# Performance work log

Measured on AMD Instinct MI355X. Metric: run time of the kernel, lower is better.

## Reference

```python
import jax, jax.numpy as jnp
import numpy as np

D_IN = 1024
D_OUT = 1024
N = 4096


def setup_inputs() -> dict:
    key = jax.random.key(0)
    kx, kq, kk, kv = jax.random.split(key, 4)
    x = jax.random.normal(kx, (N, D_IN), dtype=jnp.float32)
    # weights stored as [d_in, d_out] so that x @ W == torch Linear(x)
    s = 1.0 / np.sqrt(D_IN)
    W_q = jax.random.uniform(kq, (D_IN, D_OUT), jnp.float32, -s, s)
    W_k = jax.random.uniform(kk, (D_IN, D_OUT), jnp.float32, -s, s)
    W_v = jax.random.uniform(kv, (D_IN, D_OUT), jnp.float32, -s, s)
    return {"x": x, "W_q": W_q, "W_k": W_k, "W_v": W_v}


def reference(x, W_q, W_k, W_v):
    # x: [N, d_in]; projections -> [N, d_out]
    q = x @ W_q
    k = x @ W_k
    v = x @ W_v
    scale = 1.0 / jnp.sqrt(jnp.asarray(k.shape[-1], dtype=q.dtype))
    scores = (q @ k.T) * scale            # [N, N]
    weights = jax.nn.softmax(scores, axis=-1)
    return weights @ v                     # [N, d_out]
```

## Files before the change

### kernel.cpp

```cpp
#include <hip/hip_runtime.h>
#include <math.h>

typedef _Float16 f16;
typedef __attribute__((ext_vector_type(8))) _Float16 f16x8;
typedef __attribute__((ext_vector_type(4))) _Float16 f16x4;
typedef __attribute__((ext_vector_type(4))) float f32x4;

#define NSEQ 4096
#define DIN 1024
#define DOUT 1024

__device__ __forceinline__ void load16(const void* g, void* l) {
    __builtin_amdgcn_global_load_lds(
        (const __attribute__((address_space(1))) unsigned int*)g,
        (__attribute__((address_space(3))) unsigned int*)l, 16, 0, 0);
}

template <typename OutT, int ESUM>
__global__ __launch_bounds__(256, 2)
void gemm_bt(const f16* __restrict__ A, const f16* __restrict__ B,
             OutT* __restrict__ c0, OutT* __restrict__ c1,
             OutT* __restrict__ c2, OutT* __restrict__ c3,
             int M, int N, int K, int lda, int ldb, int ldc, float scale,
             long aStrideZ, long bStrideZ,
             f16* __restrict__ TC, int tz, int ldt, float* __restrict__ Sums)
{
    const int z = blockIdx.z;
    A += (long)z * aStrideZ;
    B += (long)z * bStrideZ;
    OutT* C = z == 0 ? c0 : (z == 1 ? c1 : (z == 2 ? c2 : c3));
    __shared__ f16 As[2 * 128 * 32];
    __shared__ f16 Bs[2 * 128 * 32];

    int gx = gridDim.x;
    int bid = blockIdx.y * gx + blockIdx.x;
    int xcd = bid & 7, s = bid >> 3;
    int px = s & 7, rest = s >> 3;
    int py = rest & 3, chunk = rest >> 2;
    int pg = xcd + (chunk << 3);
    int pcols = gx >> 3;
    int lp = 31 - __clz(pcols);
    int bx = ((pg & (pcols - 1)) << 3) + px;
    int by = ((pg >> lp) << 2) + py;

    const int t    = threadIdx.x;
    const int lane = t & 63;
    const int wave = t >> 6;
    const int wm   = (wave >> 1) * 64;
    const int wn   = (wave & 1) * 64;
    const int tile_m = by * 128;
    const int tile_n = bx * 128;
    const int quad = lane >> 4;
    const int l16  = lane & 15;
    const int srow = t >> 2;
    const int scol = ((t & 3) ^ (srow & 3)) * 8;
    const int qx8 = (quad ^ (l16 & 3)) * 8;

    f32x4 acc[4][4];
#pragma unroll
    for (int i = 0; i < 4; i++)
#pragma unroll
        for (int j = 0; j < 4; j++)
            acc[i][j] = (f32x4){0.f, 0.f, 0.f, 0.f};

    const f16* Ab = A + (long)(tile_m + srow) * lda + scol;
    const f16* Bb = B + (long)(tile_n + srow) * ldb + scol;
    f16* Asd = As + t * 8;
    f16* Bsd = Bs + t * 8;

    for (int k0 = 0; k0 < K; k0 += 64) {
        load16(Ab + k0, Asd);
        load16(Ab + (long)64 * lda + k0, Asd + 2048);
        load16(Ab + k0 + 32, Asd + 4096);
        load16(Ab + (long)64 * lda + k0 + 32, Asd + 4096 + 2048);
        load16(Bb + k0, Bsd);
        load16(Bb + (long)64 * ldb + k0, Bsd + 2048);
        load16(Bb + k0 + 32, Bsd + 4096);
        load16(Bb + (long)64 * ldb + k0 + 32, Bsd + 4096 + 2048);
        __syncthreads();
#pragma unroll
        for (int p = 0; p < 2; p++) {
            f16x8 a[4], b[4];
#pragma unroll
            for (int i = 0; i < 4; i++)
                a[i] = *(const f16x8*)(As + p * 4096 + (wm + i * 16 + l16) * 32 + qx8);
#pragma unroll
            for (int j = 0; j < 4; j++)
                b[j] = *(const f16x8*)(Bs + p * 4096 + (wn + j * 16 + l16) * 32 + qx8);
#pragma unroll
            for (int i = 0; i < 4; i++)
#pragma unroll
                for (int j = 0; j < 4; j++)
                    acc[i][j] = __builtin_amdgcn_mfma_f32_16x16x32_f16(
                        a[i], b[j], acc[i][j], 0, 0, 0);
        }
        __syncthreads();
    }
    if (TC != nullptr && z == tz) {
#pragma unroll
        for (int i = 0; i < 4; i++)
#pragma unroll
            for (int j = 0; j < 4; j++) {
                f16x4 o;
#pragma unroll
                for (int r = 0; r < 4; r++) o[r] = (f16)(acc[i][j][r] * scale);
                int row0 = tile_m + wm + i * 16 + quad * 4;
                int col  = tile_n + wn + j * 16 + l16;
                *(f16x4*)(TC + (long)col * ldt + row0) = o;
            }
    } else if (ESUM) {
        const int bxs = bx * 2 + (wn >> 6);
#pragma unroll
        for (int i = 0; i < 4; i++) {
            float rs[4] = {0.f, 0.f, 0.f, 0.f};
#pragma unroll
            for (int j = 0; j < 4; j++)
#pragma unroll
                for (int r = 0; r < 4; r++) {
                    float e = __expf(acc[i][j][r] * scale);
                    int row = tile_m + wm + i * 16 + quad * 4 + r;
                    int col = tile_n + wn + j * 16 + l16;
                    C[(long)row * ldc + col] = (OutT)e;
                    rs[r] += e;
                }
#pragma unroll
            for (int msk = 1; msk < 16; msk <<= 1)
#pragma unroll
                for (int r = 0; r < 4; r++)
                    rs[r] += __shfl_xor(rs[r], msk, 64);
            if (l16 == 0)
#pragma unroll
                for (int r = 0; r < 4; r++) {
                    int row = tile_m + wm + i * 16 + quad * 4 + r;
                    Sums[(long)row * 64 + bxs] = rs[r];
                }
        }
    } else {
#pragma unroll
        for (int i = 0; i < 4; i++)
#pragma unroll
            for (int j = 0; j < 4; j++)
#pragma unroll
                for (int r = 0; r < 4; r++) {
                    int row = tile_m + wm + i * 16 + quad * 4 + r;
                    int col = tile_n + wn + j * 16 + l16;
                    C[(long)row * ldc + col] = (OutT)(acc[i][j][r] * scale);
                }
    }
}

__global__ void prep(const float* __restrict__ x,
                     const float* __restrict__ W0, const float* __restrict__ W1,
                     const float* __restrict__ W2,
                     f16* __restrict__ xb, f16* __restrict__ Wt) {
    if (blockIdx.z == 3) {
        long base = ((long)(blockIdx.y * 16 + blockIdx.x) * 256 + threadIdx.x) * 4;
#pragma unroll
        for (int it = 0; it < 16; it++) {
            long i = base + (long)it * (256 * 256 * 4);
            f32x4 v = *(const f32x4*)(x + i);
            f16x4 o;
            o.x = (f16)v.x; o.y = (f16)v.y; o.z = (f16)v.z; o.w = (f16)v.w;
            *(f16x4*)(xb + i) = o;
        }
        return;
    }
    __shared__ f16 tile[64][65];
    const float* W = blockIdx.z == 0 ? W0 : (blockIdx.z == 1 ? W1 : W2);
    f16* O = Wt + (long)blockIdx.z * DIN * DOUT;
    int r0 = blockIdx.y * 64;
    int c0 = blockIdx.x * 64;
    int tx = threadIdx.x & 63, ty = threadIdx.x >> 6;
#pragma unroll
    for (int i = 0; i < 16; i++)
        tile[ty + i * 4][tx] = (f16)W[(long)(r0 + ty + i * 4) * DOUT + c0 + tx];
    __syncthreads();
#pragma unroll
    for (int i = 0; i < 16; i++)
        O[(long)(c0 + ty + i * 4) * DIN + r0 + tx] = tile[tx][ty + i * 4];
}

__global__ __launch_bounds__(256)
void reduce_div(const float* __restrict__ p0, const float* __restrict__ p1,
                const float* __restrict__ p2, const float* __restrict__ sums,
                float* __restrict__ out) {
    const int row = blockIdx.x;
    const int lane = threadIdx.x & 63;
    float s = sums[(long)row * 64 + lane];
#pragma unroll
    for (int msk = 1; msk < 64; msk <<= 1) s += __shfl_xor(s, msk, 64);
    const float inv = 1.f / s;
    long i = (long)row * 1024 + threadIdx.x * 4;
    f32x4 a = *(const f32x4*)(p0 + i);
    f32x4 b = *(const f32x4*)(p1 + i);
    f32x4 c = *(const f32x4*)(p2 + i);
    f32x4 d = *(const f32x4*)(out + i);
    *(f32x4*)(out + i) = ((a + b) + (c + d)) * inv;
}

extern "C" void kernel_launch(void* const* d_in, const int* in_sizes, int n_in,
                              void* d_out, int out_size, void* d_ws, size_t ws_size,
                              hipStream_t stream) {
    const float* x  = (const float*)d_in[0];
    const float* Wq = (const float*)d_in[1];
    const float* Wk = (const float*)d_in[2];
    const float* Wv = (const float*)d_in[3];
    float* out = (float*)d_out;
    char* ws = (char*)d_ws;
    const size_t MB = 1ull << 20;
    f16* xb  = (f16*)(ws);
    f16* Wt  = (f16*)(ws + 8 * MB);
    f16* Qb  = (f16*)(ws + 14 * MB);
    f16* Kb  = (f16*)(ws + 22 * MB);
    f16* Vt  = (f16*)(ws + 30 * MB);
    f16* S   = (f16*)(ws + 38 * MB);
    float* Pp0 = (float*)(ws + 70 * MB);
    float* Pp1 = (float*)(ws + 86 * MB);
    float* Pp2 = (float*)(ws + 14 * MB);
    float* Sums = (float*)(ws);

    prep<<<dim3(16, 16, 4), 256, 0, stream>>>(x, Wq, Wk, Wv, xb, Wt);
    gemm_bt<f16, 0><<<dim3(8, 32, 3), 256, 0, stream>>>(
        xb, Wt, Qb, Kb, Qb, Qb, NSEQ, DOUT, DIN, DIN, DIN, DOUT, 1.0f,
        0, (long)DIN * DOUT, Vt, 2, NSEQ, nullptr);
    gemm_bt<f16, 1><<<dim3(32, 32, 1), 256, 0, stream>>>(
        Qb, Kb, S, S, S, S, NSEQ, NSEQ, DIN, DIN, DIN, NSEQ, 0.03125f,
        0, 0, nullptr, -1, 0, Sums);
    gemm_bt<float, 0><<<dim3(8, 32, 4), 256, 0, stream>>>(
        S, Vt, Pp0, Pp1, Pp2, out, NSEQ, DOUT, 1024, NSEQ, NSEQ, DOUT, 1.0f,
        1024, 1024, nullptr, -1, 0, nullptr);
    reduce_div<<<4096, 256, 0, stream>>>(Pp0, Pp1, Pp2, Sums, out);
}
```

Baseline: 209.4 us.

## Fuse split-K reduction and softmax normalization into PV GEMM via flag handoff

The P·V GEMM now splits K two ways instead of four. The first finishing block of each tile writes its fp32 partial to scratch and sets a release flag. The second block spins on the flag, adds the partial, and applies the per-row softmax normalization computed from the Sums, writing the final output directly. This removes the separate reduce_div kernel and the extra partial-buffer traffic. In exchange it adds a memset launch and spin-waiting, and halves the grid parallelism of the last GEMM, with longer K loops per block.

```diff
diff --git a/kernel.cpp b/kernel.cpp
--- a/kernel.cpp
+++ b/kernel.cpp
@@ -16,14 +16,16 @@
         (__attribute__((address_space(3))) unsigned int*)l, 16, 0, 0);
 }
 
-template <typename OutT, int ESUM>
+template <typename OutT, int EPI>
 __global__ __launch_bounds__(256, 2)
 void gemm_bt(const f16* __restrict__ A, const f16* __restrict__ B,
              OutT* __restrict__ c0, OutT* __restrict__ c1,
              OutT* __restrict__ c2, OutT* __restrict__ c3,
              int M, int N, int K, int lda, int ldb, int ldc, float scale,
              long aStrideZ, long bStrideZ,
-             f16* __restrict__ TC, int tz, int ldt, float* __restrict__ Sums)
+             f16* __restrict__ TC, int tz, int ldt,
+             float* __restrict__ Sums, float* __restrict__ scratch,
+             int* __restrict__ flags)
 {
     const int z = blockIdx.z;
     A += (long)z * aStrideZ;
@@ -96,19 +98,32 @@
         }
         __syncthreads();
     }
-    if (TC != nullptr && z == tz) {
-#pragma unroll
-        for (int i = 0; i < 4; i++)
-#pragma unroll
-            for (int j = 0; j < 4; j++) {
-                f16x4 o;
-#pragma unroll
-                for (int r = 0; r < 4; r++) o[r] = (f16)(acc[i][j][r] * scale);
-                int row0 = tile_m + wm + i * 16 + quad * 4;
-                int col  = tile_n + wn + j * 16 + l16;
-                *(f16x4*)(TC + (long)col * ldt + row0) = o;
-            }
-    } else if (ESUM) {
+    if (EPI == 1) {
+        if (z == tz) {
+#pragma unroll
+            for (int i = 0; i < 4; i++)
+#pragma unroll
+                for (int j = 0; j < 4; j++) {
+                    f16x4 o;
+#pragma unroll
+                    for (int r = 0; r < 4; r++) o[r] = (f16)(acc[i][j][r] * scale);
+                    int row0 = tile_m + wm + i * 16 + quad * 4;
+                    int col  = tile_n + wn + j * 16 + l16;
+                    *(f16x4*)(TC + (long)col * ldt + row0) = o;
+                }
+        } else {
+#pragma unroll
+            for (int i = 0; i < 4; i++)
+#pragma unroll
+                for (int j = 0; j < 4; j++)
+#pragma unroll
+                    for (int r = 0; r < 4; r++) {
+                        int row = tile_m + wm + i * 16 + quad * 4 + r;
+                        int col = tile_n + wn + j * 16 + l16;
+                        C[(long)row * ldc + col] = (OutT)(acc[i][j][r] * scale);
+                    }
+        }
+    } else if (EPI == 2) {
         const int bxs = bx * 2 + (wn >> 6);
 #pragma unroll
         for (int i = 0; i < 4; i++) {
@@ -135,17 +150,68 @@
                     Sums[(long)row * 64 + bxs] = rs[r];
                 }
         }
-    } else {
-#pragma unroll
-        for (int i = 0; i < 4; i++)
-#pragma unroll
-            for (int j = 0; j < 4; j++)
-#pragma unroll
-                for (int r = 0; r < 4; r++) {
-                    int row = tile_m + wm + i * 16 + quad * 4 + r;
-                    int col = tile_n + wn + j * 16 + l16;
-                    C[(long)row * ldc + col] = (OutT)(acc[i][j][r] * scale);
-                }
+    } else if (EPI == 3) {
+        const int tile = by * 8 + bx;
+        __shared__ int role_s;
+        if (t == 0) role_s = atomicAdd(&flags[2 * tile], 1);
+        __syncthreads();
+        float* scr = scratch + (long)tile * (128 * 128);
+        if (role_s == 0) {
+#pragma unroll
+            for (int i = 0; i < 4; i++)
+#pragma unroll
+                for (int j = 0; j < 4; j++)
+#pragma unroll
+                    for (int r = 0; r < 4; r++) {
+                        int ri = wm + i * 16 + quad * 4 + r;
+                        int ci = wn + j * 16 + l16;
+                        __hip_atomic_store(&scr[ri * 128 + ci], acc[i][j][r],
+                                           __ATOMIC_RELAXED,
+                                           __HIP_MEMORY_SCOPE_AGENT);
+                    }
+            __syncthreads();
+            __threadfence();
+            if (t == 0)
+                __hip_atomic_store(&flags[2 * tile + 1], 1, __ATOMIC_RELEASE,
+                                   __HIP_MEMORY_SCOPE_AGENT);
+        } else {
+            float* invl = (float*)As;
+            {
+                float sv[32];
+                const int rbase = wave * 32;
+#pragma unroll
+                for (int r = 0; r < 32; r++)
+                    sv[r] = Sums[(long)(tile_m + rbase + r) * 64 + lane];
+#pragma unroll
+                for (int r = 0; r < 32; r++) {
+                    float sm = sv[r];
+#pragma unroll
+                    for (int msk = 1; msk < 64; msk <<= 1)
+                        sm += __shfl_xor(sm, msk, 64);
+                    if (lane == 0) invl[rbase + r] = 1.f / sm;
+                }
+            }
+            if (t == 0)
+                while (__hip_atomic_load(&flags[2 * tile + 1], __ATOMIC_ACQUIRE,
+                                         __HIP_MEMORY_SCOPE_AGENT) == 0)
+                    __builtin_amdgcn_s_sleep(2);
+            __syncthreads();
+            float* Co = (float*)c0;
+#pragma unroll
+            for (int i = 0; i < 4; i++)
+#pragma unroll
+                for (int j = 0; j < 4; j++)
+#pragma unroll
+                    for (int r = 0; r < 4; r++) {
+                        int ri = wm + i * 16 + quad * 4 + r;
+                        int ci = wn + j * 16 + l16;
+                        float p = __hip_atomic_load(&scr[ri * 128 + ci],
+                                                    __ATOMIC_RELAXED,
+                                                    __HIP_MEMORY_SCOPE_AGENT);
+                        Co[(long)(tile_m + ri) * ldc + tile_n + ci] =
+                            (acc[i][j][r] + p) * invl[ri];
+                    }
+        }
     }
 }
 
@@ -178,24 +244,6 @@
 #pragma unroll
     for (int i = 0; i < 16; i++)
         O[(long)(c0 + ty + i * 4) * DIN + r0 + tx] = tile[tx][ty + i * 4];
-}
-
-__global__ __launch_bounds__(256)
-void reduce_div(const float* __restrict__ p0, const float* __restrict__ p1,
-                const float* __restrict__ p2, const float* __restrict__ sums,
-                float* __restrict__ out) {
-    const int row = blockIdx.x;
-    const int lane = threadIdx.x & 63;
-    float s = sums[(long)row * 64 + lane];
-#pragma unroll
-    for (int msk = 1; msk < 64; msk <<= 1) s += __shfl_xor(s, msk, 64);
-    const float inv = 1.f / s;
-    long i = (long)row * 1024 + threadIdx.x * 4;
-    f32x4 a = *(const f32x4*)(p0 + i);
-    f32x4 b = *(const f32x4*)(p1 + i);
-    f32x4 c = *(const f32x4*)(p2 + i);
-    f32x4 d = *(const f32x4*)(out + i);
-    *(f32x4*)(out + i) = ((a + b) + (c + d)) * inv;
 }
 
 extern "C" void kernel_launch(void* const* d_in, const int* in_sizes, int n_in,
@@ -214,20 +262,19 @@
     f16* Kb  = (f16*)(ws + 22 * MB);
     f16* Vt  = (f16*)(ws + 30 * MB);
     f16* S   = (f16*)(ws + 38 * MB);
-    float* Pp0 = (float*)(ws + 70 * MB);
-    float* Pp1 = (float*)(ws + 86 * MB);
-    float* Pp2 = (float*)(ws + 14 * MB);
-    float* Sums = (float*)(ws);
-
+    float* Sums    = (float*)(ws);
+    float* scratch = (float*)(ws + 14 * MB);
+    int*   flags   = (int*)(ws + 70 * MB);
+
+    hipMemsetAsync(flags, 0, 2048, stream);
     prep<<<dim3(16, 16, 4), 256, 0, stream>>>(x, Wq, Wk, Wv, xb, Wt);
-    gemm_bt<f16, 0><<<dim3(8, 32, 3), 256, 0, stream>>>(
+    gemm_bt<f16, 1><<<dim3(8, 32, 3), 256, 0, stream>>>(
         xb, Wt, Qb, Kb, Qb, Qb, NSEQ, DOUT, DIN, DIN, DIN, DOUT, 1.0f,
-        0, (long)DIN * DOUT, Vt, 2, NSEQ, nullptr);
-    gemm_bt<f16, 1><<<dim3(32, 32, 1), 256, 0, stream>>>(
+        0, (long)DIN * DOUT, Vt, 2, NSEQ, nullptr, nullptr, nullptr);
+    gemm_bt<f16, 2><<<dim3(32, 32, 1), 256, 0, stream>>>(
         Qb, Kb, S, S, S, S, NSEQ, NSEQ, DIN, DIN, DIN, NSEQ, 0.03125f,
-        0, 0, nullptr, -1, 0, Sums);
-    gemm_bt<float, 0><<<dim3(8, 32, 4), 256, 0, stream>>>(
-        S, Vt, Pp0, Pp1, Pp2, out, NSEQ, DOUT, 1024, NSEQ, NSEQ, DOUT, 1.0f,
-        1024, 1024, nullptr, -1, 0, nullptr);
-    reduce_div<<<4096, 256, 0, stream>>>(Pp0, Pp1, Pp2, Sums, out);
-}
+        0, 0, nullptr, -1, 0, Sums, nullptr, nullptr);
+    gemm_bt<float, 3><<<dim3(8, 32, 2), 256, 0, stream>>>(
+        S, Vt, out, out, out, out, NSEQ, DOUT, 2048, NSEQ, NSEQ, DOUT, 1.0f,
+        2048, 2048, nullptr, -1, 0, Sums, scratch, flags);
+}
```

Result: slower. 224.1 us (+7.0%).
